# Kernel tuning notes

Measured on AMD Instinct MI355X. Metric: run time of the kernel, lower is better.

## Reference

```python
import jax, jax.numpy as jnp
import numpy as np

N = 2048      # num_nodes (padded graph size)
D = 128       # node_embedding_dim
E = 8         # edge_embedding_dim (num learned edge-type channels)
ITERS = 8     # GGNN iterations (shared weights)


def setup_inputs() -> dict:
    key = jax.random.key(0)
    ks = jax.random.split(key, 8)
    s = 1.0 / np.sqrt(D)
    return {
        "node_embeddings": jax.random.normal(ks[0], (N, D), jnp.float32),
        # dense edge tensor; scaled by 1/N so the sum-over-senders message
        # aggregation stays O(1) in magnitude (real graphs are sparse)
        "edge_embeddings": jax.random.uniform(ks[1], (N, N, E), jnp.float32) / N,
        "W_msg": jax.random.normal(ks[2], (E, D, D), jnp.float32) * s,
        "b_msg": jnp.zeros((D,), jnp.float32),
        "Wi": jax.random.normal(ks[3], (D, 3 * D), jnp.float32) * s,
        "Wh": jax.random.normal(ks[4], (D, 3 * D), jnp.float32) * s,
        "b_gru": jnp.zeros((3 * D,), jnp.float32),
        "A_readout": jax.random.normal(ks[5], (D, D), jnp.float32) * s,
    }


def reference(node_embeddings, edge_embeddings, W_msg, b_msg, Wi, Wh, b_gru, A_readout):
    """GGNN steps (LinearMessagePassing + GRU update, weights shared via scan)
    followed by pairwise bilinear edge readout -> [N, N] logits."""

    def step(h, _):
        # per-edge-type linear transform of sender embeddings: [N, E, D]
        per_edge = jnp.einsum('sd,edh->seh', h, W_msg)
        # aggregate over senders weighted by dense edge tensor: [N, D]
        messages = jnp.einsum('ste,seh->th', edge_embeddings, per_edge) + b_msg
        # gated recurrent (GRU) update: state = node embeddings, input = messages
        gi = messages @ Wi + b_gru            # [N, 3D]
        gh = h @ Wh                           # [N, 3D]
        i_r, i_z, i_n = jnp.split(gi, 3, axis=-1)
        h_r, h_z, h_n = jnp.split(gh, 3, axis=-1)
        r = jax.nn.sigmoid(i_r + h_r)
        z = jax.nn.sigmoid(i_z + h_z)
        n = jnp.tanh(i_n + r * h_n)
        h_new = (1.0 - z) * n + z * h
        return h_new, None

    h, _ = jax.lax.scan(step, node_embeddings, None, length=ITERS)
    # bilinear pairwise readout -> weighted adjacency logits [N, N]
    logits = jnp.einsum('id,de,je->ij', h, A_readout, h)
    return logits
```

## Files before the change

### kernel.cpp

```cpp
#include <hip/hip_runtime.h>
#include <math.h>
#include <stdint.h>

#define Nn 2048
#define Dd 128
#define Ee 8
#define NIT 8
#define KT (Nn*Ee)
#define KSPLIT 16

typedef __bf16 bf16;
typedef __attribute__((ext_vector_type(8))) __bf16 bf16x8;
typedef __attribute__((ext_vector_type(4))) __bf16 bf16x4;
typedef __attribute__((ext_vector_type(4))) float f32x4;
typedef __attribute__((ext_vector_type(16))) float f32x16;

__device__ __forceinline__ f32x4 mfma16(bf16x8 a, bf16x8 b, f32x4 c){
    return __builtin_amdgcn_mfma_f32_16x16x32_bf16(a, b, c, 0, 0, 0);
}
__device__ __forceinline__ f32x16 mfma32(bf16x8 a, bf16x8 b, f32x16 c){
    return __builtin_amdgcn_mfma_f32_32x32x16_bf16(a, b, c, 0, 0, 0);
}
__device__ __forceinline__ void g2lds16(const void* g, void* l){
    __builtin_amdgcn_global_load_lds((const uint32_t*)g, (uint32_t*)l, 16, 0, 0);
}

__global__ __launch_bounds__(256) void k_prep(
    const float* __restrict__ node, const float* __restrict__ Wmsg,
    const float* __restrict__ Wi,   const float* __restrict__ Wh,
    const float* __restrict__ Ar,
    float* __restrict__ h32, bf16* __restrict__ hb,
    bf16* __restrict__ WmT, bf16* __restrict__ WiT, bf16* __restrict__ WhT,
    bf16* __restrict__ ArT)
{
    int tid = blockIdx.x*256 + threadIdx.x;
    int stride = gridDim.x*256;
    for (int i = tid; i < Nn*Dd; i += stride){
        float v = node[i]; h32[i] = v; hb[i] = (bf16)v;
    }
    for (int i = tid; i < Ee*Dd*Dd; i += stride){
        int e = i >> 14; int r = i & 16383; int h = r >> 7; int d = r & 127;
        WmT[i] = (bf16)Wmsg[e*Dd*Dd + d*Dd + h];
    }
    for (int i = tid; i < 384*Dd; i += stride){
        int j = i >> 7; int d = i & 127;
        WiT[i] = (bf16)Wi[d*384 + j];
        WhT[i] = (bf16)Wh[d*384 + j];
    }
    for (int i = tid; i < Dd*Dd; i += stride){
        int h = i >> 7; int d = i & 127;
        ArT[i] = (bf16)Ar[d*Dd + h];
    }
}

__global__ __launch_bounds__(256) void k_prep_edge(
    const float* __restrict__ edge, bf16* __restrict__ edge_bf)
{
    const size_t total = (size_t)Nn*Nn*Ee;
    size_t base = ((size_t)blockIdx.x*256 + threadIdx.x)*8;
    size_t stride = (size_t)gridDim.x*256*8;
    for (size_t i = base; i < total; i += stride){
        f32x4 v0 = *(const f32x4*)&edge[i];
        f32x4 v1 = *(const f32x4*)&edge[i+4];
        bf16x8 o;
        for (int j = 0; j < 4; j++){ o[j] = (bf16)v0[j]; o[j+4] = (bf16)v1[j]; }
        *(bf16x8*)&edge_bf[i] = o;
    }
}

__global__ __launch_bounds__(256) void k_per_edge(
    const bf16* __restrict__ hb, const bf16* __restrict__ WmT,
    bf16* __restrict__ Pt)
{
    __shared__ bf16 Blds[Ee][16][Dd+8];
    const int s0 = blockIdx.x * 64;
    const int h0 = blockIdx.y * 16;
    const int tid = threadIdx.x;
    for (int i = 0; i < 8; i++){
        int idx = tid + i*256;
        int e = idx >> 8, row = (idx >> 4) & 15, c = idx & 15;
        *(bf16x8*)&Blds[e][row][c*8] =
            *(const bf16x8*)&WmT[e*Dd*Dd + (h0+row)*Dd + c*8];
    }
    __syncthreads();
    const int lane = tid & 63, wave = tid >> 6;
    const int quad = lane >> 4, l16 = lane & 15;
    const int srow = s0 + wave*16 + l16;
    f32x4 acc[Ee];
    for (int e = 0; e < Ee; e++) acc[e] = (f32x4){0.f,0.f,0.f,0.f};
    for (int kk = 0; kk < 4; kk++){
        int k0 = kk*32 + quad*8;
        bf16x8 a = *(const bf16x8*)&hb[srow*Dd + k0];
        for (int e = 0; e < Ee; e++){
            bf16x8 b = *(const bf16x8*)&Blds[e][l16][k0];
            acc[e] = mfma16(a, b, acc[e]);
        }
    }
    const int h = h0 + l16;
    for (int r = 0; r < 4; r++){
        int s = s0 + wave*16 + quad*4 + r;
        bf16x8 po;
        for (int e = 0; e < Ee; e++) po[e] = (bf16)acc[e][r];
        *(bf16x8*)&Pt[((size_t)s*Dd + h)*Ee] = po;
    }
}

__global__ __launch_bounds__(256, 1) void k_msg_gemm(
    const bf16* __restrict__ edge_bf, const bf16* __restrict__ Pt,
    float* __restrict__ msgP)
{
    __shared__ __align__(16) char ldsb[3*32768];
    const int flat = blockIdx.y*16 + blockIdx.x;
    const int by = (flat & 7)*2 + ((flat >> 3) & 1);
    const int bx = flat >> 4;
    const int t0 = bx * 128;
    const int sblk = by * 128;
    const int tid = threadIdx.x;
    const int lane = tid & 63, wave = tid >> 6;
    const int half = lane >> 5, l31 = lane & 31;
    const int trow = t0 + wave*32 + l31;
    const char* Ptb = (const char*)Pt;

    f32x16 acc[4];
    #pragma unroll
    for (int nt = 0; nt < 4; nt++)
        for (int i = 0; i < 16; i++) acc[nt][i] = 0.f;

    bf16x8 A[3][8];

#define STAGE(ch_) do{                                                         \
    const char* _src = Ptb + (size_t)(sblk + (ch_)*16)*2048                    \
                           + wave*1024 + lane*16;                              \
    char* _dst = ldsb + ((ch_)%3)*32768 + wave*1024;                           \
    _Pragma("unroll")                                                          \
    for (int j = 0; j < 8; j++)                                                \
        g2lds16(_src + j*4096, _dst + j*4096);                                 \
}while(0)

#define PREF(ch_) do{                                                         \
    int _sc = sblk + (ch_)*16 + half;                                          \
    _Pragma("unroll")                                                          \
    for (int ks = 0; ks < 8; ks++)                                             \
        A[(ch_)%3][ks] = *(const bf16x8*)&edge_bf[(size_t)(_sc + ks*2)*16384 + trow*8]; \
}while(0)

#define COMPUTE(ch_) do{                                                       \
    const bf16* _bt = (const bf16*)(ldsb + ((ch_)%3)*32768);                   \
    _Pragma("unroll")                                                          \
    for (int ks = 0; ks < 8; ks++){                                            \
        const bf16* _bp = _bt + (ks*2 + half)*1024 + l31*8;                    \
        acc[0] = mfma32(A[(ch_)%3][ks], *(const bf16x8*)(_bp      ), acc[0]);  \
        acc[1] = mfma32(A[(ch_)%3][ks], *(const bf16x8*)(_bp + 256), acc[1]);  \
        acc[2] = mfma32(A[(ch_)%3][ks], *(const bf16x8*)(_bp + 512), acc[2]);  \
        acc[3] = mfma32(A[(ch_)%3][ks], *(const bf16x8*)(_bp + 768), acc[3]);  \
    }                                                                          \
}while(0)

#define STEP(ch_, wcnt_, dostage_) do{                                         \
    asm volatile("s_waitcnt vmcnt(" #wcnt_ ")" ::: "memory");                  \
    __builtin_amdgcn_s_barrier();                                              \
    COMPUTE(ch_);                                                              \
    __builtin_amdgcn_s_barrier();                                              \
    if (dostage_){ STAGE((ch_)+3); PREF((ch_)+3); }                            \
}while(0)

    STAGE(0); PREF(0);
    STAGE(1); PREF(1);
    STAGE(2); PREF(2);

    STEP(0, 32, 1);
    STEP(1, 32, 1);
    STEP(2, 32, 1);
    STEP(3, 32, 1);
    STEP(4, 32, 1);
    STEP(5, 32, 0);
    STEP(6, 16, 0);
    STEP(7,  0, 0);

#undef STAGE
#undef PREF
#undef COMPUTE
#undef STEP

    float* dst = msgP + (size_t)by*(Nn*Dd);
    #pragma unroll
    for (int nt = 0; nt < 4; nt++){
        int h = nt*32 + l31;
        #pragma unroll
        for (int r = 0; r < 16; r++){
            int row = (r&3) + 8*(r>>2) + 4*half;
            dst[(size_t)(t0 + wave*32 + row)*Dd + h] = acc[nt][r];
        }
    }
}

__global__ __launch_bounds__(256) void k_update(
    const float* __restrict__ msgP, const float* __restrict__ bmsg,
    const bf16* __restrict__ WiT,  const bf16* __restrict__ WhT,
    const float* __restrict__ bgru, const bf16* __restrict__ WmT,
    float* __restrict__ h32, bf16* __restrict__ hb, bf16* __restrict__ Pt)
{
    __shared__ __align__(16) bf16 msg_b[16][152];
    __shared__ __align__(16) bf16 h_b[16][152];
    __shared__ __align__(16) bf16 hn_b[16][152];
    __shared__ __align__(16) float Gi[8][388];
    __shared__ __align__(16) float Gh[8][388];

    const int t0 = blockIdx.x * 8;
    const int tid = threadIdx.x;
    const int lane = tid & 63, wave = tid >> 6;
    const int quad = lane >> 4, l16 = lane & 15;

    for (int i = tid; i < 8*152; i += 256){
        (&msg_b[8][0])[i] = (bf16)0.f;
        (&h_b [8][0])[i] = (bf16)0.f;
        (&hn_b[8][0])[i] = (bf16)0.f;
    }

    {
        int m = tid >> 5;
        int d0 = (tid & 31) * 4;
        f32x4 s = *(const f32x4*)&bmsg[d0];
        #pragma unroll
        for (int p = 0; p < KSPLIT; p++)
            s += *(const f32x4*)&msgP[((size_t)p*Nn + t0 + m)*Dd + d0];
        for (int j = 0; j < 4; j++) msg_b[m][d0+j] = (bf16)s[j];
        *(bf16x4*)&h_b[m][d0] = *(const bf16x4*)&hb[(t0+m)*Dd + d0];
    }
    __syncthreads();

    {
        f32x4 accA[12];
        #pragma unroll
        for (int i = 0; i < 12; i++) accA[i] = (f32x4){0.f,0.f,0.f,0.f};
        #pragma unroll
        for (int kk = 0; kk < 4; kk++){
            int k0 = kk*32 + quad*8;
            bf16x8 aGi = *(const bf16x8*)&msg_b[l16][k0];
            bf16x8 aGh = *(const bf16x8*)&h_b[l16][k0];
            #pragma unroll
            for (int i = 0; i < 12; i++){
                int tile = wave*12 + i;
                int isGi = tile < 24;
                int jt = isGi ? tile : tile - 24;
                const bf16* WT = isGi ? WiT : WhT;
                bf16x8 b = *(const bf16x8*)&WT[(jt*16 + l16)*Dd + k0];
                accA[i] = mfma16(isGi ? aGi : aGh, b, accA[i]);
            }
        }
        #pragma unroll
        for (int i = 0; i < 12; i++){
            int tile = wave*12 + i;
            int jt = tile < 24 ? tile : tile - 24;
            float* G = tile < 24 ? &Gi[0][0] : &Gh[0][0];
            #pragma unroll
            for (int r = 0; r < 4; r++){
                int row = quad*4 + r;
                if (row < 8) G[row*388 + jt*16 + l16] = accA[i][r];
            }
        }
    }
    __syncthreads();

    {
        int m = tid >> 5;
        int d0 = (tid & 31) * 4;
        f32x4 gir = *(const f32x4*)&Gi[m][d0];
        f32x4 giz = *(const f32x4*)&Gi[m][128+d0];
        f32x4 gin = *(const f32x4*)&Gi[m][256+d0];
        f32x4 ghr = *(const f32x4*)&Gh[m][d0];
        f32x4 ghz = *(const f32x4*)&Gh[m][128+d0];
        f32x4 ghn = *(const f32x4*)&Gh[m][256+d0];
        f32x4 bR = *(const f32x4*)&bgru[d0];
        f32x4 bZ = *(const f32x4*)&bgru[128+d0];
        f32x4 bN = *(const f32x4*)&bgru[256+d0];
        f32x4 ho = *(const f32x4*)&h32[(t0+m)*Dd + d0];
        f32x4 hnv; bf16x4 hb4;
        for (int j = 0; j < 4; j++){
            float r = 1.f / (1.f + expf(-(gir[j] + ghr[j] + bR[j])));
            float z = 1.f / (1.f + expf(-(giz[j] + ghz[j] + bZ[j])));
            float n = tanhf(gin[j] + bN[j] + r * ghn[j]);
            hnv[j] = (1.f - z) * n + z * ho[j];
            hb4[j] = (bf16)hnv[j];
        }
        *(f32x4*)&h32[(t0+m)*Dd + d0] = hnv;
        *(bf16x4*)&hb[(t0+m)*Dd + d0] = hb4;
        *(bf16x4*)&hn_b[m][d0] = hb4;
    }
    __syncthreads();

    {
        f32x4 accP[2][8];
        #pragma unroll
        for (int i = 0; i < 2; i++)
            for (int e = 0; e < 8; e++) accP[i][e] = (f32x4){0.f,0.f,0.f,0.f};
        #pragma unroll
        for (int kk = 0; kk < 4; kk++){
            int k0 = kk*32 + quad*8;
            bf16x8 a = *(const bf16x8*)&hn_b[l16][k0];
            #pragma unroll
            for (int i = 0; i < 2; i++){
                int th = wave*2 + i;
                #pragma unroll
                for (int e = 0; e < 8; e++){
                    bf16x8 b = *(const bf16x8*)&WmT[e*Dd*Dd + (th*16 + l16)*Dd + k0];
                    accP[i][e] = mfma16(a, b, accP[i][e]);
                }
            }
        }
        #pragma unroll
        for (int i = 0; i < 2; i++){
            int h = (wave*2 + i)*16 + l16;
            #pragma unroll
            for (int r = 0; r < 4; r++){
                int s = quad*4 + r;
                if (s < 8){
                    bf16x8 po;
                    for (int e = 0; e < 8; e++) po[e] = (bf16)accP[i][e][r];
                    *(bf16x8*)&Pt[((size_t)(t0 + s)*Dd + h)*Ee] = po;
                }
            }
        }
    }
}

__global__ __launch_bounds__(256) void k_read1(
    const bf16* __restrict__ hb, const bf16* __restrict__ ArT, bf16* __restrict__ t1)
{
    __shared__ bf16 Blds[Dd][Dd+8];
    const int s0 = blockIdx.x * 64;
    const int tid = threadIdx.x;
    for (int i = 0; i < 8; i++){
        int idx = tid + i*256; int row = idx >> 4, c = idx & 15;
        *(bf16x8*)&Blds[row][c*8] = *(const bf16x8*)&ArT[row*Dd + c*8];
    }
    __syncthreads();
    const int lane = tid & 63, wave = tid >> 6;
    const int quad = lane >> 4, l16 = lane & 15;
    const int srow = s0 + wave*16 + l16;
    f32x4 acc[8];
    for (int nt = 0; nt < 8; nt++) acc[nt] = (f32x4){0.f,0.f,0.f,0.f};
    for (int kk = 0; kk < 4; kk++){
        int k0 = kk*32 + quad*8;
        bf16x8 a = *(const bf16x8*)&hb[srow*Dd + k0];
        for (int nt = 0; nt < 8; nt++){
            bf16x8 b = *(const bf16x8*)&Blds[nt*16 + l16][k0];
            acc[nt] = mfma16(a, b, acc[nt]);
        }
    }
    for (int nt = 0; nt < 8; nt++){
        int h = nt*16 + l16;
        for (int r = 0; r < 4; r++){
            int s = s0 + wave*16 + quad*4 + r;
            t1[s*Dd + h] = (bf16)acc[nt][r];
        }
    }
}

__global__ __launch_bounds__(256) void k_read2(
    const bf16* __restrict__ t1, const bf16* __restrict__ hb, float* __restrict__ out)
{
    const int i0 = blockIdx.x * 64, j0 = blockIdx.y * 128;
    const int tid = threadIdx.x;
    const int lane = tid & 63, wave = tid >> 6;
    const int quad = lane >> 4, l16 = lane & 15;
    const int irow = i0 + wave*16 + l16;
    f32x4 acc[8];
    for (int nt = 0; nt < 8; nt++) acc[nt] = (f32x4){0.f,0.f,0.f,0.f};
    for (int kk = 0; kk < 4; kk++){
        int k0 = kk*32 + quad*8;
        bf16x8 a = *(const bf16x8*)&t1[irow*Dd + k0];
        for (int nt = 0; nt < 8; nt++){
            int j = j0 + nt*16 + l16;
            bf16x8 b = *(const bf16x8*)&hb[j*Dd + k0];
            acc[nt] = mfma16(a, b, acc[nt]);
        }
    }
    for (int nt = 0; nt < 8; nt++){
        int j = j0 + nt*16 + l16;
        for (int r = 0; r < 4; r++){
            int irw = i0 + wave*16 + quad*4 + r;
            out[(size_t)irw*Nn + j] = acc[nt][r];
        }
    }
}

extern "C" void kernel_launch(void* const* d_in, const int* in_sizes, int n_in,
                              void* d_out, int out_size, void* d_ws, size_t ws_size,
                              hipStream_t stream)
{
    const float* node = (const float*)d_in[0];
    const float* edge = (const float*)d_in[1];
    const float* Wmsg = (const float*)d_in[2];
    const float* bmsg = (const float*)d_in[3];
    const float* Wi   = (const float*)d_in[4];
    const float* Wh   = (const float*)d_in[5];
    const float* bgru = (const float*)d_in[6];
    const float* Ar   = (const float*)d_in[7];
    float* out = (float*)d_out;

    char* ws = (char*)d_ws;
    bf16*  edge_bf = (bf16*)ws;          ws += (size_t)Nn*Nn*Ee*2;
    float* msgP = (float*)ws;            ws += (size_t)KSPLIT*Nn*Dd*4;
    bf16*  Pt  = (bf16*)ws;              ws += (size_t)Dd*KT*2;
    float* h32 = (float*)ws;             ws += (size_t)Nn*Dd*4;
    bf16*  hb  = (bf16*)ws;              ws += (size_t)Nn*Dd*2;
    bf16*  WmT = (bf16*)ws;              ws += (size_t)Ee*Dd*Dd*2;
    bf16*  WiT = (bf16*)ws;              ws += (size_t)384*Dd*2;
    bf16*  WhT = (bf16*)ws;              ws += (size_t)384*Dd*2;
    bf16*  ArT = (bf16*)ws;              ws += (size_t)Dd*Dd*2;
    bf16*  t1  = (bf16*)ws;              ws += (size_t)Nn*Dd*2;

    k_prep<<<dim3(256), 256, 0, stream>>>(node, Wmsg, Wi, Wh, Ar,
                                          h32, hb, WmT, WiT, WhT, ArT);
    k_prep_edge<<<dim3(4096), 256, 0, stream>>>(edge, edge_bf);
    k_per_edge<<<dim3(32, 8), 256, 0, stream>>>(hb, WmT, Pt);
    for (int it = 0; it < NIT; it++){
        k_msg_gemm<<<dim3(16,16), 256, 0, stream>>>(edge_bf, Pt, msgP);
        k_update  <<<dim3(256),   256, 0, stream>>>(msgP, bmsg, WiT, WhT, bgru,
                                                    WmT, h32, hb, Pt);
    }
    k_read1<<<dim3(32),     256, 0, stream>>>(hb, ArT, t1);
    k_read2<<<dim3(32, 16), 256, 0, stream>>>(t1, hb, out);
}
```

Before: 628.4 us.

## Fuse edge fp32-to-bf16 conversion into first message GEMM and double-buffer

Removes the separate edge conversion kernel. The first-iteration message GEMM now reads fp32 edges directly, converts them in registers, uses them, and writes the bf16 copy for later iterations. This saves one full write-then-read pass over the 64 MB bf16 edge tensor. The GEMM pipeline also changes from a 3-stage buffer with partial vmcnt waits to 2-stage double buffering with full waits, which frees LDS and registers but may expose more load latency.

```diff
diff --git a/kernel.cpp b/kernel.cpp
--- a/kernel.cpp
+++ b/kernel.cpp
@@ -50,21 +50,6 @@
     for (int i = tid; i < Dd*Dd; i += stride){
         int h = i >> 7; int d = i & 127;
         ArT[i] = (bf16)Ar[d*Dd + h];
-    }
-}
-
-__global__ __launch_bounds__(256) void k_prep_edge(
-    const float* __restrict__ edge, bf16* __restrict__ edge_bf)
-{
-    const size_t total = (size_t)Nn*Nn*Ee;
-    size_t base = ((size_t)blockIdx.x*256 + threadIdx.x)*8;
-    size_t stride = (size_t)gridDim.x*256*8;
-    for (size_t i = base; i < total; i += stride){
-        f32x4 v0 = *(const f32x4*)&edge[i];
-        f32x4 v1 = *(const f32x4*)&edge[i+4];
-        bf16x8 o;
-        for (int j = 0; j < 4; j++){ o[j] = (bf16)v0[j]; o[j+4] = (bf16)v1[j]; }
-        *(bf16x8*)&edge_bf[i] = o;
     }
 }
 
@@ -105,11 +90,12 @@
     }
 }
 
-__global__ __launch_bounds__(256, 1) void k_msg_gemm(
-    const bf16* __restrict__ edge_bf, const bf16* __restrict__ Pt,
-    float* __restrict__ msgP)
-{
-    __shared__ __align__(16) char ldsb[3*32768];
+template<int FIRST>
+__global__ __launch_bounds__(256) void k_msg_gemm(
+    const float* __restrict__ edge_f, bf16* __restrict__ edge_bf,
+    const bf16* __restrict__ Pt, float* __restrict__ msgP)
+{
+    __shared__ __align__(16) char ldsb[65536];
     const int flat = blockIdx.y*16 + blockIdx.x;
     const int by = (flat & 7)*2 + ((flat >> 3) & 1);
     const int bx = flat >> 4;
@@ -126,61 +112,69 @@
     for (int nt = 0; nt < 4; nt++)
         for (int i = 0; i < 16; i++) acc[nt][i] = 0.f;
 
-    bf16x8 A[3][8];
+    bf16x8 A0[8], A1[8];
 
 #define STAGE(ch_) do{                                                         \
     const char* _src = Ptb + (size_t)(sblk + (ch_)*16)*2048                    \
                            + wave*1024 + lane*16;                              \
-    char* _dst = ldsb + ((ch_)%3)*32768 + wave*1024;                           \
+    char* _dst = ldsb + ((ch_)&1)*32768 + wave*1024;                           \
     _Pragma("unroll")                                                          \
     for (int j = 0; j < 8; j++)                                                \
         g2lds16(_src + j*4096, _dst + j*4096);                                 \
 }while(0)
 
-#define PREF(ch_) do{                                                         \
+#define PREF(AD_, ch_) do{                                                     \
     int _sc = sblk + (ch_)*16 + half;                                          \
     _Pragma("unroll")                                                          \
-    for (int ks = 0; ks < 8; ks++)                                             \
-        A[(ch_)%3][ks] = *(const bf16x8*)&edge_bf[(size_t)(_sc + ks*2)*16384 + trow*8]; \
+    for (int ks = 0; ks < 8; ks++){                                            \
+        size_t _off = (size_t)(_sc + ks*2)*16384 + trow*8;                     \
+        if (FIRST){                                                            \
+            f32x4 _v0 = *(const f32x4*)&edge_f[_off];                          \
+            f32x4 _v1 = *(const f32x4*)&edge_f[_off+4];                        \
+            bf16x8 _o;                                                         \
+            for (int _j = 0; _j < 4; _j++){                                    \
+                _o[_j] = (bf16)_v0[_j]; _o[_j+4] = (bf16)_v1[_j];              \
+            }                                                                  \
+            AD_[ks] = _o;                                                      \
+            *(bf16x8*)&edge_bf[_off] = _o;                                     \
+        } else {                                                               \
+            AD_[ks] = *(const bf16x8*)&edge_bf[_off];                          \
+        }                                                                      \
+    }                                                                          \
 }while(0)
 
-#define COMPUTE(ch_) do{                                                       \
-    const bf16* _bt = (const bf16*)(ldsb + ((ch_)%3)*32768);                   \
+#define COMPUTE(AD_, ch_) do{                                                  \
+    const bf16* _bt = (const bf16*)(ldsb + ((ch_)&1)*32768);                   \
     _Pragma("unroll")                                                          \
     for (int ks = 0; ks < 8; ks++){                                            \
         const bf16* _bp = _bt + (ks*2 + half)*1024 + l31*8;                    \
-        acc[0] = mfma32(A[(ch_)%3][ks], *(const bf16x8*)(_bp      ), acc[0]);  \
-        acc[1] = mfma32(A[(ch_)%3][ks], *(const bf16x8*)(_bp + 256), acc[1]);  \
-        acc[2] = mfma32(A[(ch_)%3][ks], *(const bf16x8*)(_bp + 512), acc[2]);  \
-        acc[3] = mfma32(A[(ch_)%3][ks], *(const bf16x8*)(_bp + 768), acc[3]);  \
+        acc[0] = mfma32(AD_[ks], *(const bf16x8*)(_bp      ), acc[0]);         \
+        acc[1] = mfma32(AD_[ks], *(const bf16x8*)(_bp + 256), acc[1]);         \
+        acc[2] = mfma32(AD_[ks], *(const bf16x8*)(_bp + 512), acc[2]);         \
+        acc[3] = mfma32(AD_[ks], *(const bf16x8*)(_bp + 768), acc[3]);         \
     }                                                                          \
 }while(0)
 
-#define STEP(ch_, wcnt_, dostage_) do{                                         \
-    asm volatile("s_waitcnt vmcnt(" #wcnt_ ")" ::: "memory");                  \
-    __builtin_amdgcn_s_barrier();                                              \
-    COMPUTE(ch_);                                                              \
-    __builtin_amdgcn_s_barrier();                                              \
-    if (dostage_){ STAGE((ch_)+3); PREF((ch_)+3); }                            \
-}while(0)
-
-    STAGE(0); PREF(0);
-    STAGE(1); PREF(1);
-    STAGE(2); PREF(2);
-
-    STEP(0, 32, 1);
-    STEP(1, 32, 1);
-    STEP(2, 32, 1);
-    STEP(3, 32, 1);
-    STEP(4, 32, 1);
-    STEP(5, 32, 0);
-    STEP(6, 16, 0);
-    STEP(7,  0, 0);
-
+    STAGE(0); PREF(A0, 0);
+    asm volatile("s_waitcnt vmcnt(0)" ::: "memory");
+    __syncthreads();
+    #pragma unroll
+    for (int cc = 0; cc < 4; cc++){
+        const int ch = cc*2;
+        STAGE(ch+1); PREF(A1, ch+1);
+        COMPUTE(A0, ch);
+        asm volatile("s_waitcnt vmcnt(0)" ::: "memory");
+        __syncthreads();
+        if (ch+2 < 8){ STAGE(ch+2); PREF(A0, ch+2); }
+        COMPUTE(A1, ch+1);
+        if (ch+2 < 8){
+            asm volatile("s_waitcnt vmcnt(0)" ::: "memory");
+            __syncthreads();
+        }
+    }
 #undef STAGE
 #undef PREF
 #undef COMPUTE
-#undef STEP
 
     float* dst = msgP + (size_t)by*(Nn*Dd);
     #pragma unroll
@@ -413,12 +407,14 @@
 
     k_prep<<<dim3(256), 256, 0, stream>>>(node, Wmsg, Wi, Wh, Ar,
                                           h32, hb, WmT, WiT, WhT, ArT);
-    k_prep_edge<<<dim3(4096), 256, 0, stream>>>(edge, edge_bf);
     k_per_edge<<<dim3(32, 8), 256, 0, stream>>>(hb, WmT, Pt);
     for (int it = 0; it < NIT; it++){
-        k_msg_gemm<<<dim3(16,16), 256, 0, stream>>>(edge_bf, Pt, msgP);
-        k_update  <<<dim3(256),   256, 0, stream>>>(msgP, bmsg, WiT, WhT, bgru,
-                                                    WmT, h32, hb, Pt);
+        if (it == 0)
+            k_msg_gemm<1><<<dim3(16,16), 256, 0, stream>>>(edge, edge_bf, Pt, msgP);
+        else
+            k_msg_gemm<0><<<dim3(16,16), 256, 0, stream>>>(edge, edge_bf, Pt, msgP);
+        k_update<<<dim3(256), 256, 0, stream>>>(msgP, bmsg, WiT, WhT, bgru,
+                                                WmT, h32, hb, Pt);
     }
     k_read1<<<dim3(32),     256, 0, stream>>>(hb, ArT, t1);
     k_read2<<<dim3(32, 16), 256, 0, stream>>>(t1, hb, out);
```

After: 619.7 us. No clear change (-1.4%).
